# Optimization experiments

Hardware: AMD Instinct MI355X
Metric: run time of the kernel (lower is better)

## Reference

```python
import jax, jax.numpy as jnp
import numpy as np

D = 256  # api_embed_channels
B = 8    # number of graphs
N = 128  # invoked APIs per graph (nodes); edges = N*N (fully connected incl. self-loops)
V = 10000


def setup_inputs() -> dict:
    key = jax.random.key(0)
    ks = jax.random.split(key, 12)
    s = 0.02
    return {
        "Xs": jax.random.normal(ks[0], (B, D), jnp.float32),
        "api_embeds": jax.random.normal(ks[1], (V, D), jnp.float32),
        "W1": jax.random.normal(ks[2], (2 * D, D), jnp.float32) * s,
        "b1": jnp.zeros((D,), jnp.float32),
        "W2": jax.random.normal(ks[3], (2 * D, D), jnp.float32) * s,
        "b2": jnp.zeros((D,), jnp.float32),
        "W3": jax.random.normal(ks[4], (2 * D, D), jnp.float32) * s,
        "b3": jnp.zeros((D,), jnp.float32),
        "W4": jax.random.normal(ks[5], (2 * D, 1), jnp.float32) * s,
        "b4": jnp.zeros((1,), jnp.float32),
        "invoked": jax.random.randint(ks[6], (B, N), 0, V, jnp.int32),
    }


def reference(Xs, api_embeds, W1, b1, W2, b2, W3, b3, W4, b4, invoked):
    # Gather invoked-API node features per graph: [B, N, D]
    feat = api_embeds[invoked]
    # Fully connected edge list in DGL insertion order: edge i -> (u=i//N, v=i%N).
    # src feats vary along axis 1 (u), dst feats along axis 2 (v).
    src = jnp.broadcast_to(feat[:, :, None, :], (B, N, N, D))
    dst = jnp.broadcast_to(feat[:, None, :, :], (B, N, N, D))
    # n2v_mlp1 per edge: Linear(2D -> D) on cat([src, dst])
    m = jnp.concatenate([src, dst], axis=-1) @ W1 + b1          # [B, N, N, D]
    # mean aggregation over incoming edges of dst v == mean over u (axis 1)
    e2n1 = jnp.mean(m, axis=1)                                   # [B, N, D]
    # n2n_mlp2: Linear(2D -> D) on cat([feat, e2n1])
    h = jnp.concatenate([feat, e2n1], axis=-1) @ W2 + b2         # [B, N, D]
    # n2v_mlp3 per edge: Linear(2D -> D) on cat([h_src, h_dst])
    hs = jnp.broadcast_to(h[:, :, None, :], (B, N, N, D))
    hd = jnp.broadcast_to(h[:, None, :, :], (B, N, N, D))
    ef = jnp.concatenate([hs, hd], axis=-1) @ W3 + b3            # [B, N, N, D]
    ef = ef.reshape(B, N * N, D)                                 # edge order u*N + v
    # edge_exist_mlp on cat([ef, x repeated per edge]): Linear(2D -> 1) + sigmoid
    x = jnp.broadcast_to(Xs[:, None, :], (B, N * N, D))
    logits = jnp.concatenate([ef, x], axis=-1) @ W4 + b4         # [B, N*N, 1]
    return jax.nn.sigmoid(logits)
```

## Files before the change

kernel.cpp:

```cpp
#include <hip/hip_runtime.h>


__device__ __forceinline__ float wred(float v) {
#pragma unroll
  for (int o = 32; o > 0; o >>= 1) v += __shfl_xor(v, o, 64);
  return v;
}
__device__ __forceinline__ float dot4(float4 a, float4 b) {
  return a.x * b.x + a.y * b.y + a.z * b.z + a.w * b.w;
}

#define OFF_PM   0
#define OFF_WA   131328
#define OFF_WB   131584
#define OFF_VA   131840
#define OFF_VB   132096
#define OFF_QS   132352
#define OFF_C0   132608
#define OFF_CALL 132616

__global__ __launch_bounds__(256) void k1(
    const float* __restrict__ Xs,
    const float* __restrict__ W1, const float* __restrict__ b1,
    const float* __restrict__ W2, const float* __restrict__ b2,
    const float* __restrict__ W3, const float* __restrict__ b3,
    const float* __restrict__ W4, const float* __restrict__ b4,
    float* __restrict__ ws) {
  const int blk = blockIdx.x, tid = threadIdx.x;
  float* PM = ws + OFF_PM;
  const float* W2bot = W2 + 256 * 256;
  __shared__ float w1s[8][256];
  __shared__ float4 part[8][4][64];

  if (blk < 64) {
    const int r0 = blk * 8;
    const int c4 = tid & 63, wv = tid >> 6;
#pragma unroll
    for (int i = 0; i < 8; ++i)
      ((float*)w1s)[i * 256 + tid] = W1[(size_t)r0 * 256 + i * 256 + tid];
    __syncthreads();
    const float4* w2b4 = (const float4*)W2bot;
    float4 acc[8];
#pragma unroll
    for (int i = 0; i < 8; ++i) acc[i] = make_float4(0.f, 0.f, 0.f, 0.f);
    const int kb = wv * 64;
#pragma unroll 4
    for (int i = 0; i < 64; ++i) {
      int k = kb + i;
      float4 w = w2b4[k * 64 + c4];
#pragma unroll
      for (int r = 0; r < 8; ++r) {
        float x = w1s[r][k];
        acc[r].x += x * w.x; acc[r].y += x * w.y;
        acc[r].z += x * w.z; acc[r].w += x * w.w;
      }
    }
#pragma unroll
    for (int r = 0; r < 8; ++r) part[r][wv][c4] = acc[r];
    __syncthreads();
#pragma unroll
    for (int j = 0; j < 2; ++j) {
      int item = tid + j * 256;
      int row = item >> 6, c = item & 63;
      float4 p0 = part[row][0][c], p1 = part[row][1][c];
      float4 p2 = part[row][2][c], p3 = part[row][3][c];
      float4 s = make_float4(p0.x + p1.x + p2.x + p3.x,
                             p0.y + p1.y + p2.y + p3.y,
                             p0.z + p1.z + p2.z + p3.z,
                             p0.w + p1.w + p2.w + p3.w);
      int r = r0 + row;
      if (r >= 256) {
        float4 t = ((const float4*)(W2 + (size_t)(r - 256) * 256))[c];
        s.x += t.x; s.y += t.y; s.z += t.z; s.w += t.w;
      }
      ((float4*)(PM + (size_t)r * 256))[c] = s;
    }
  } else if (blk < 192) {
    const int lane = tid & 63, wv = tid >> 6;
    const int t = (blk - 64) * 4 + wv;
    float4 w4a = ((const float4*)W4)[lane];
    float4 rv = ((const float4*)(W3 + (size_t)t * 256))[lane];
    float s = wred(dot4(rv, w4a));
    if (lane == 0) {
      if (t < 256) ws[OFF_WA + t] = s; else ws[OFF_WB + t - 256] = s;
    }
  } else {
    const int lane = tid & 63, wv = tid >> 6;
    float4 w4a = ((const float4*)W4)[lane];
    float4 w4b4 = ((const float4*)W4)[lane + 64];
    float sb3 = wred(dot4(((const float4*)b3)[lane], w4a));
    for (int bi = wv; bi < 8; bi += 4) {
      float xd = wred(dot4(((const float4*)(Xs + (size_t)bi * 256))[lane], w4b4));
      if (lane == 0) ws[OFF_C0 + bi] = b4[0] + sb3 + xd;
    }
    const int c4 = tid & 63, rg = tid >> 6;
    const float4* w2b4 = (const float4*)W2bot;
    float4 acc = make_float4(0.f, 0.f, 0.f, 0.f);
#pragma unroll 8
    for (int i = 0; i < 64; ++i) {
      int k = rg * 64 + i;
      float4 w = w2b4[k * 64 + c4];
      float bv = b1[k];
      acc.x += bv * w.x; acc.y += bv * w.y; acc.z += bv * w.z; acc.w += bv * w.w;
    }
    part[0][rg][c4] = acc;
    __syncthreads();
    if (tid < 64) {
      float4 p0 = part[0][0][tid], p1 = part[0][1][tid];
      float4 p2 = part[0][2][tid], p3 = part[0][3][tid];
      float4 bb = ((const float4*)b2)[tid];
      float4 s = make_float4(p0.x + p1.x + p2.x + p3.x + bb.x,
                             p0.y + p1.y + p2.y + p3.y + bb.y,
                             p0.z + p1.z + p2.z + p3.z + bb.z,
                             p0.w + p1.w + p2.w + p3.w + bb.w);
      ((float4*)(PM + (size_t)512 * 256))[tid] = s;
    }
  }
}

__global__ __launch_bounds__(256) void k2(float* __restrict__ ws) {
  const int blk = blockIdx.x, tid = threadIdx.x;
  const int lane = tid & 63, wv = tid >> 6;
  const float* PM = ws + OFF_PM;
  float4 wa4 = ((const float4*)(ws + OFF_WA))[lane];
  float4 wb4 = ((const float4*)(ws + OFF_WB))[lane];
  if (blk < 128) {
    const int t = blk * 4 + wv;
    if (t < 256) {
      float4 rv = ((const float4*)(PM + (size_t)(256 + t) * 256))[lane];
      float sa = wred(dot4(rv, wa4));
      float sb = wred(dot4(rv, wb4));
      if (lane == 0) { ws[OFF_VA + t] = sa; ws[OFF_VB + t] = sb; }
    } else {
      float4 rv = ((const float4*)(PM + (size_t)(t - 256) * 256))[lane];
      float4 s4 = make_float4(wa4.x + wb4.x, wa4.y + wb4.y,
                              wa4.z + wb4.z, wa4.w + wb4.w);
      float s = wred(dot4(rv, s4));
      if (lane == 0) ws[OFF_QS + t - 256] = s;
    }
  } else {
    __shared__ float sAllSh;
    if (wv == 0) {
      float4 rv = ((const float4*)(PM + (size_t)512 * 256))[lane];
      float4 s4 = make_float4(wa4.x + wb4.x, wa4.y + wb4.y,
                              wa4.z + wb4.z, wa4.w + wb4.w);
      float s = wred(dot4(rv, s4));
      if (lane == 0) sAllSh = s;
    }
    __syncthreads();
    if (tid < 8) ws[OFF_CALL + tid] = ws[OFF_C0 + tid] + sAllSh;
  }
}

__global__ __launch_bounds__(1024) void k3(
    const float* __restrict__ api, const int* __restrict__ invoked,
    const float* __restrict__ ws, float* __restrict__ out) {
  const int g = blockIdx.x >> 3, sub = blockIdx.x & 7;
  const int tid = threadIdx.x;
  const int lane = tid & 63, wv = tid >> 6;
  __shared__ alignas(16) float Ash[128], Bsh[128], scsh[128];
  __shared__ float CbSh;

  float4 f[8];
  const int ub = wv * 8;
  int idx[8];
#pragma unroll
  for (int i = 0; i < 8; ++i) idx[i] = invoked[(g << 7) + ub + i];
#pragma unroll
  for (int i = 0; i < 8; ++i)
    f[i] = ((const float4*)(api + (size_t)idx[i] * 256))[lane];

  float4 va4 = ((const float4*)(ws + OFF_VA))[lane];
  float4 vb4 = ((const float4*)(ws + OFF_VB))[lane];
  float4 q4  = ((const float4*)(ws + OFF_QS))[lane];
#pragma unroll
  for (int i = 0; i < 8; ++i) {
    float sa = wred(dot4(f[i], va4));
    float sb = wred(dot4(f[i], vb4));
    float sc = wred(dot4(f[i], q4));
    if (lane == 0) { Ash[ub + i] = sa; Bsh[ub + i] = sb; scsh[ub + i] = sc; }
  }
  __syncthreads();
  if (wv == 0) {
    float t = scsh[lane] + scsh[lane + 64];
    t = wred(t);
    if (lane == 0) CbSh = t * (1.f / 128.f) + ws[OFF_CALL + g];
  }
  __syncthreads();
  const float Cb = CbSh;
  if (tid < 512) {
    int u = (sub << 4) + (tid >> 5);
    int v4 = tid & 31;
    float a = Ash[u] + Cb;
    float4 bv = ((const float4*)Bsh)[v4];
    float4 r;
    r.x = 1.f / (1.f + __expf(-(a + bv.x)));
    r.y = 1.f / (1.f + __expf(-(a + bv.y)));
    r.z = 1.f / (1.f + __expf(-(a + bv.z)));
    r.w = 1.f / (1.f + __expf(-(a + bv.w)));
    ((float4*)(out + (g << 14) + (u << 7)))[v4] = r;
  }
}

extern "C" void kernel_launch(void* const* d_in, const int* in_sizes, int n_in,
                              void* d_out, int out_size, void* d_ws, size_t ws_size,
                              hipStream_t stream) {
  const float* Xs  = (const float*)d_in[0];
  const float* api = (const float*)d_in[1];
  const float* W1  = (const float*)d_in[2];
  const float* b1  = (const float*)d_in[3];
  const float* W2  = (const float*)d_in[4];
  const float* b2  = (const float*)d_in[5];
  const float* W3  = (const float*)d_in[6];
  const float* b3  = (const float*)d_in[7];
  const float* W4  = (const float*)d_in[8];
  const float* b4  = (const float*)d_in[9];
  const int* invoked = (const int*)d_in[10];
  float* out = (float*)d_out;
  float* ws = (float*)d_ws;

  hipLaunchKernelGGL(k1, dim3(193), dim3(256), 0, stream,
                     Xs, W1, b1, W2, b2, W3, b3, W4, b4, ws);
  hipLaunchKernelGGL(k2, dim3(129), dim3(256), 0, stream, ws);
  hipLaunchKernelGGL(k3, dim3(64), dim3(1024), 0, stream,
                     api, invoked, ws, out);
}
```

Before: 22.91 us.

## Fuse k2 into k3 with redundant per-block matvec over bf16 PM

```diff
diff --git a/kernel.cpp b/kernel.cpp
--- a/kernel.cpp
+++ b/kernel.cpp
@@ -9,15 +9,20 @@
 __device__ __forceinline__ float dot4(float4 a, float4 b) {
   return a.x * b.x + a.y * b.y + a.z * b.z + a.w * b.w;
 }
-
-#define OFF_PM   0
-#define OFF_WA   131328
-#define OFF_WB   131584
-#define OFF_VA   131840
-#define OFF_VB   132096
-#define OFF_QS   132352
-#define OFF_C0   132608
-#define OFF_CALL 132616
+__device__ __forceinline__ unsigned short f2bf(float x) {
+  union { float f; unsigned int u; } v; v.f = x;
+  unsigned int r = (v.u + 0x7fffu + ((v.u >> 16) & 1u)) >> 16;
+  return (unsigned short)r;
+}
+__device__ __forceinline__ float bf2f(unsigned short h) {
+  union { unsigned int u; float f; } v; v.u = ((unsigned int)h) << 16;
+  return v.f;
+}
+
+#define PMH_ROWS 513
+#define OFF_WA   65664
+#define OFF_WB   (OFF_WA + 256)
+#define OFF_C0   (OFF_WB + 256)
 
 __global__ __launch_bounds__(256) void k1(
     const float* __restrict__ Xs,
@@ -27,7 +32,7 @@
     const float* __restrict__ W4, const float* __restrict__ b4,
     float* __restrict__ ws) {
   const int blk = blockIdx.x, tid = threadIdx.x;
-  float* PM = ws + OFF_PM;
+  unsigned short* PMh = (unsigned short*)ws;
   const float* W2bot = W2 + 256 * 256;
   __shared__ float w1s[8][256];
   __shared__ float4 part[8][4][64];
@@ -73,7 +78,9 @@
         float4 t = ((const float4*)(W2 + (size_t)(r - 256) * 256))[c];
         s.x += t.x; s.y += t.y; s.z += t.z; s.w += t.w;
       }
-      ((float4*)(PM + (size_t)r * 256))[c] = s;
+      ushort4 h;
+      h.x = f2bf(s.x); h.y = f2bf(s.y); h.z = f2bf(s.z); h.w = f2bf(s.w);
+      ((ushort4*)(PMh + (size_t)r * 256))[c] = h;
     }
   } else if (blk < 192) {
     const int lane = tid & 63, wv = tid >> 6;
@@ -113,53 +120,23 @@
                              p0.y + p1.y + p2.y + p3.y + bb.y,
                              p0.z + p1.z + p2.z + p3.z + bb.z,
                              p0.w + p1.w + p2.w + p3.w + bb.w);
-      ((float4*)(PM + (size_t)512 * 256))[tid] = s;
-    }
-  }
-}
-
-__global__ __launch_bounds__(256) void k2(float* __restrict__ ws) {
-  const int blk = blockIdx.x, tid = threadIdx.x;
-  const int lane = tid & 63, wv = tid >> 6;
-  const float* PM = ws + OFF_PM;
-  float4 wa4 = ((const float4*)(ws + OFF_WA))[lane];
-  float4 wb4 = ((const float4*)(ws + OFF_WB))[lane];
-  if (blk < 128) {
-    const int t = blk * 4 + wv;
-    if (t < 256) {
-      float4 rv = ((const float4*)(PM + (size_t)(256 + t) * 256))[lane];
-      float sa = wred(dot4(rv, wa4));
-      float sb = wred(dot4(rv, wb4));
-      if (lane == 0) { ws[OFF_VA + t] = sa; ws[OFF_VB + t] = sb; }
-    } else {
-      float4 rv = ((const float4*)(PM + (size_t)(t - 256) * 256))[lane];
-      float4 s4 = make_float4(wa4.x + wb4.x, wa4.y + wb4.y,
-                              wa4.z + wb4.z, wa4.w + wb4.w);
-      float s = wred(dot4(rv, s4));
-      if (lane == 0) ws[OFF_QS + t - 256] = s;
-    }
-  } else {
-    __shared__ float sAllSh;
-    if (wv == 0) {
-      float4 rv = ((const float4*)(PM + (size_t)512 * 256))[lane];
-      float4 s4 = make_float4(wa4.x + wb4.x, wa4.y + wb4.y,
-                              wa4.z + wb4.z, wa4.w + wb4.w);
-      float s = wred(dot4(rv, s4));
-      if (lane == 0) sAllSh = s;
-    }
-    __syncthreads();
-    if (tid < 8) ws[OFF_CALL + tid] = ws[OFF_C0 + tid] + sAllSh;
-  }
-}
-
-__global__ __launch_bounds__(1024) void k3(
+      ushort4 h;
+      h.x = f2bf(s.x); h.y = f2bf(s.y); h.z = f2bf(s.z); h.w = f2bf(s.w);
+      ((ushort4*)(PMh + (size_t)512 * 256))[tid] = h;
+    }
+  }
+}
+
+__global__ __launch_bounds__(1024) void k23(
     const float* __restrict__ api, const int* __restrict__ invoked,
     const float* __restrict__ ws, float* __restrict__ out) {
   const int g = blockIdx.x >> 3, sub = blockIdx.x & 7;
   const int tid = threadIdx.x;
   const int lane = tid & 63, wv = tid >> 6;
+  const unsigned short* PMh = (const unsigned short*)ws;
+  __shared__ alignas(16) float qsL[256], vaL[256], vbL[256];
   __shared__ alignas(16) float Ash[128], Bsh[128], scsh[128];
-  __shared__ float CbSh;
+  __shared__ float CbSh, sAllSh;
 
   float4 f[8];
   const int ub = wv * 8;
@@ -170,9 +147,32 @@
   for (int i = 0; i < 8; ++i)
     f[i] = ((const float4*)(api + (size_t)idx[i] * 256))[lane];
 
-  float4 va4 = ((const float4*)(ws + OFF_VA))[lane];
-  float4 vb4 = ((const float4*)(ws + OFF_VB))[lane];
-  float4 q4  = ((const float4*)(ws + OFF_QS))[lane];
+  float4 wa4 = ((const float4*)(ws + OFF_WA))[lane];
+  float4 wb4 = ((const float4*)(ws + OFF_WB))[lane];
+  float4 sm4 = make_float4(wa4.x + wb4.x, wa4.y + wb4.y,
+                           wa4.z + wb4.z, wa4.w + wb4.w);
+#pragma unroll 4
+  for (int t = wv; t < 513; t += 16) {
+    ushort4 h = ((const ushort4*)(PMh + (size_t)t * 256))[lane];
+    float4 m = make_float4(bf2f(h.x), bf2f(h.y), bf2f(h.z), bf2f(h.w));
+    if (t < 256) {
+      float s = wred(dot4(m, sm4));
+      if (lane == 0) qsL[t] = s;
+    } else if (t < 512) {
+      float sa = dot4(m, wa4);
+      float sb = dot4(m, wb4);
+      sa = wred(sa); sb = wred(sb);
+      if (lane == 0) { vaL[t - 256] = sa; vbL[t - 256] = sb; }
+    } else {
+      float s = wred(dot4(m, sm4));
+      if (lane == 0) sAllSh = s;
+    }
+  }
+  __syncthreads();
+
+  float4 va4 = ((const float4*)vaL)[lane];
+  float4 vb4 = ((const float4*)vbL)[lane];
+  float4 q4  = ((const float4*)qsL)[lane];
 #pragma unroll
   for (int i = 0; i < 8; ++i) {
     float sa = wred(dot4(f[i], va4));
@@ -184,7 +184,7 @@
   if (wv == 0) {
     float t = scsh[lane] + scsh[lane + 64];
     t = wred(t);
-    if (lane == 0) CbSh = t * (1.f / 128.f) + ws[OFF_CALL + g];
+    if (lane == 0) CbSh = t * (1.f / 128.f) + ws[OFF_C0 + g] + sAllSh;
   }
   __syncthreads();
   const float Cb = CbSh;
@@ -221,7 +221,6 @@
 
   hipLaunchKernelGGL(k1, dim3(193), dim3(256), 0, stream,
                      Xs, W1, b1, W2, b2, W3, b3, W4, b4, ws);
-  hipLaunchKernelGGL(k2, dim3(129), dim3(256), 0, stream, ws);
-  hipLaunchKernelGGL(k3, dim3(64), dim3(1024), 0, stream,
+  hipLaunchKernelGGL(k23, dim3(64), dim3(1024), 0, stream,
                      api, invoked, ws, out);
 }
```

Result: slower. 41.44 us (+80.9%).
